# Kernel tuning notes

Hardware: AMD Instinct MI355X
Metric: run time of the kernel (lower is better)

Reference implementation:

```python
import jax, jax.numpy as jnp
import numpy as np

B, S = 2, 256
CN, CE = 256, 128        # node / edge channels
A, H, V = 32, 8, 32      # attention_size, heads, value_size
AH, VH = A * H, V * H


def setup_inputs() -> dict:
    key = jax.random.key(0)
    ks = jax.random.split(key, 16)
    w = lambda k, shape: (jax.random.normal(k, shape) * 0.05).astype(jnp.float32)
    nodes = jax.random.normal(ks[0], (B, CN, S), dtype=jnp.float32)
    edges = jax.random.normal(ks[1], (B, CE, S, S), dtype=jnp.float32)
    lengths = jnp.array([S, (3 * S) // 4])            # padded-batch valid lengths
    mask = jnp.arange(S)[None, :] < lengths[:, None]  # (B, S) bool
    return dict(
        nodes=nodes, edges=edges, mask=mask,
        Wq=w(ks[2], (AH, CN)),
        Wk=w(ks[3], (AH, CN + CE)),
        Wv=w(ks[4], (VH, CN + CE)),
        Wo=w(ks[5], (CN, VH)),
        We=w(ks[6], (CE, VH + CE)),
        Wm1=w(ks[7], (CN, CN)), bm1=jnp.zeros((CN,), jnp.float32),
        Wm2=w(ks[8], (CN, CN)), bm2=jnp.zeros((CN,), jnp.float32),
        We1=w(ks[9], (CE, CE)), be1=jnp.zeros((CE,), jnp.float32),
        We2=w(ks[10], (CE, CE)), be2=jnp.zeros((CE,), jnp.float32),
        an0=(jax.random.normal(ks[11], (CN,)) * 0.1).astype(jnp.float32),
        an1=(jax.random.normal(ks[12], (CN,)) * 0.1).astype(jnp.float32),
        ae0=(jax.random.normal(ks[13], (CE,)) * 0.1).astype(jnp.float32),
        ae1=(jax.random.normal(ks[14], (CE,)) * 0.1).astype(jnp.float32),
    )


def _block(nodes, edges, mask, Wq, Wk, Wv, Wo, We,
           Wm1, bm1, Wm2, bm2, We1, be1, We2, be2, an0, an1, ae0, ae1):
    relu = jax.nn.relu
    b, _, s = nodes.shape
    # node MLP (1x1 conv, ReLU, 1x1 conv, ReLU) + ReZero residual; dropout in eval mode = identity
    h = relu(jnp.einsum('oc,bcs->bos', Wm1, nodes) + bm1[None, :, None])
    h = relu(jnp.einsum('oc,bcs->bos', Wm2, h) + bm2[None, :, None])
    nodes = nodes + an0[None, :, None] * h
    # edge MLP (1x1 conv2d) + ReZero residual
    g = relu(jnp.einsum('oc,bcij->boij', We1, edges) + be1[None, :, None, None])
    g = relu(jnp.einsum('oc,bcij->boij', We2, g) + be2[None, :, None, None])
    edges = edges + ae0[None, :, None, None] * g
    # materialized multi-head attention
    q = jnp.einsum('ac,bcs->bas', Wq, nodes).reshape(b, H, A, s)            # (B,H,A,S)
    ne = jnp.concatenate([jnp.broadcast_to(nodes[:, :, :, None], (b, CN, s, s)), edges], axis=1)
    k = jnp.einsum('ac,bcij->baij', Wk, ne).reshape(b, H, A, s, s)          # (B,H,A,S,S)
    v = jnp.einsum('vc,bcij->bvij', Wv, ne).reshape(b, H, V, s, s)          # (B,H,V,S,S)
    sim = jnp.einsum('bhai,bhaij->bhij', q, k) / jnp.sqrt(jnp.float32(A))   # (B,H,S,S)
    sim = jnp.where(mask[:, None, None, :], sim, jnp.float32(-1e9))
    sim = jax.nn.softmax(sim, axis=-1)
    mm = (mask[:, None, None, :] & mask[:, None, :, None]).astype(sim.dtype)  # (B,1,S,S)
    sim = sim * mm
    v = v * mm[:, None]
    nf = jnp.einsum('bhij,bhvij->bhvi', sim, v).reshape(b, H * V, s)        # (B,HV,S)
    node_att = jnp.einsum('oc,bcs->bos', Wo, nf)
    # edge features: broadcast node features along j, symmetrize via transpose+average
    ef = 0.5 * (nf[:, :, :, None] + nf[:, :, None, :])                      # (B,HV,S,S)
    edge_att = jnp.einsum('oc,bcij->boij', We, jnp.concatenate([ef, edges], axis=1))
    # ReZero residuals (project_* are Identity since in_size == out_size)
    nodes = nodes + an1[None, :, None] * node_att
    edges = edges + ae1[None, :, None, None] * edge_att
    # final masking
    nodes = nodes * mask[:, None, :].astype(nodes.dtype)
    edges = edges * mm
    return nodes, edges


def reference(nodes, edges, mask, Wq, Wk, Wv, Wo, We, Wm1, bm1, Wm2, bm2,
              We1, be1, We2, be2, an0, an1, ae0, ae1):
    return _block(nodes, edges, mask, Wq, Wk, Wv, Wo, We,
                  Wm1, bm1, Wm2, bm2, We1, be1, We2, be2, an0, an1, ae0, ae1)
```

## Files before the change

kernel.cpp:

```cpp
#include <hip/hip_runtime.h>
#include <hip/hip_bf16.h>
#include <cstdint>
#include <cstddef>

constexpr int B_  = 2;
constexpr int S_  = 256;
constexpr int CN_ = 256;
constexpr int CE_ = 128;
constexpr int A_  = 32;
constexpr int H_  = 8;
constexpr int V_  = 32;
constexpr int AH_ = A_ * H_;
constexpr int VH_ = V_ * H_;
constexpr int SS_ = S_ * S_;
constexpr int CNE_ = CN_ + CE_;

constexpr size_t OFF_N1   = 0;
constexpr size_t OFF_Q    = OFF_N1  + (size_t)B_*CN_*S_;
constexpr size_t OFF_VN   = OFF_Q   + (size_t)B_*AH_*S_;
constexpr size_t OFF_NF   = OFF_VN  + (size_t)B_*VH_*S_;
constexpr size_t OFF_WNF  = OFF_NF  + (size_t)B_*VH_*S_;
constexpr size_t OFF_SE   = OFF_WNF + (size_t)B_*CE_*S_;
constexpr size_t OFF_QW   = OFF_SE  + (size_t)B_*S_*1024;
constexpr size_t OFF_WB1  = OFF_QW  + (size_t)B_*S_*1024;
constexpr size_t OFF_WB2  = OFF_WB1 + 16384;
constexpr size_t OFF_WBE  = OFF_WB2 + 16384;
constexpr size_t OFF_MASK = OFF_WBE + 16384;

__device__ inline uint16_t f2bf(float x) {
    uint32_t u = __float_as_uint(x);
    uint32_t r = (u + 0x7fffu + ((u >> 16) & 1u)) >> 16;
    return (uint16_t)r;
}
__device__ inline float bf2f(uint16_t h) {
    return __uint_as_float(((uint32_t)h) << 16);
}
__device__ inline uint32_t pack_split(float v) {
    uint32_t u  = __float_as_uint(v);
    uint32_t hm = u & 0xffff0000u;
    return hm | (__float_as_uint(v - __uint_as_float(hm)) >> 16);
}
__device__ inline float unpack_f32(uint32_t p) {
    return __uint_as_float(p & 0xffff0000u) + __uint_as_float(p << 16);
}

typedef __attribute__((ext_vector_type(8))) short sh8;
typedef __attribute__((ext_vector_type(4))) short sh4;
typedef __attribute__((ext_vector_type(4))) float f32x4;

#define MFMA_B16(a, b, c) __builtin_amdgcn_mfma_f32_16x16x32_bf16((a), (b), (c), 0, 0, 0)

__device__ inline int eidx(int j, int c) {
    return (j * 136 + c) ^ (((j >> 3) & 7) << 3);
}

#define GEMM4_K256(WROW, XS, A0, A1, A2, A3)                                   \
    for (int c = 0; c < 256; c += 4) {                                         \
        float4 w  = *(const float4*)((WROW) + c);                              \
        float4 x0 = *(const float4*)((XS) + (c+0)*4);                          \
        float4 x1 = *(const float4*)((XS) + (c+1)*4);                          \
        float4 x2 = *(const float4*)((XS) + (c+2)*4);                          \
        float4 x3 = *(const float4*)((XS) + (c+3)*4);                          \
        A0 = fmaf(w.x,x0.x,fmaf(w.y,x1.x,fmaf(w.z,x2.x,fmaf(w.w,x3.x,A0))));   \
        A1 = fmaf(w.x,x0.y,fmaf(w.y,x1.y,fmaf(w.z,x2.y,fmaf(w.w,x3.y,A1))));   \
        A2 = fmaf(w.x,x0.z,fmaf(w.y,x1.z,fmaf(w.z,x2.z,fmaf(w.w,x3.z,A2))));   \
        A3 = fmaf(w.x,x0.w,fmaf(w.y,x1.w,fmaf(w.z,x2.w,fmaf(w.w,x3.w,A3))));   \
    }

__global__ void k_mask_norm(const unsigned char* __restrict__ mraw,
                            float* __restrict__ ws)
{
    int t = threadIdx.x;
    unsigned char b1 = mraw[1], b2 = mraw[2];
    float mv;
    if (b1 == (unsigned char)1) {
        mv = mraw[t] ? 1.f : 0.f;
    } else if (b2 == (unsigned char)128) {
        mv = (((const float*)mraw)[t] != 0.f) ? 1.f : 0.f;
    } else {
        mv = (((const int*)mraw)[t] != 0) ? 1.f : 0.f;
    }
    ws[OFF_MASK + t] = mv;
}

__global__ void k_wprep(const float* __restrict__ We1_,
                        const float* __restrict__ We2_,
                        const float* __restrict__ We_,
                        float* __restrict__ ws)
{
    int idx = blockIdx.x * 256 + threadIdx.x;
    int m = idx >> 14;
    int r = idx & 16383;
    int o = r >> 7, c = r & 127;
    ushort* wb1 = (ushort*)(ws + OFF_WB1);
    ushort* wb2 = (ushort*)(ws + OFF_WB2);
    ushort* wbe = (ushort*)(ws + OFF_WBE);
    if (m == 0)      wb1[r] = f2bf(We1_[o*CE_ + c]);
    else if (m == 1) wb2[r] = f2bf(We2_[o*CE_ + c]);
    else             wbe[r] = f2bf(We_[o*CNE_ + CN_ + c]);
}

__global__ __launch_bounds__(256)
void k_node_mlp_qv(const float* __restrict__ nodes,
                   const float* __restrict__ Wm1, const float* __restrict__ bm1,
                   const float* __restrict__ Wm2, const float* __restrict__ bm2,
                   const float* __restrict__ an0,
                   const float* __restrict__ Wq,  const float* __restrict__ Wv,
                   float* __restrict__ ws)
{
    __shared__ float xs[CN_ * 4];
    __shared__ float hs[CN_ * 4];
    const int t  = threadIdx.x;
    const int b  = blockIdx.x >> 6;
    const int s0 = (blockIdx.x & 63) * 4;

    {
        float4 nv = *(const float4*)(nodes + (size_t)(b*CN_+t)*S_ + s0);
        xs[t*4+0]=nv.x; xs[t*4+1]=nv.y; xs[t*4+2]=nv.z; xs[t*4+3]=nv.w;
    }
    __syncthreads();

    float a0, a1, a2, a3;
    {
        float bv = bm1[t]; a0=bv; a1=bv; a2=bv; a3=bv;
        GEMM4_K256(Wm1 + t*CN_, xs, a0, a1, a2, a3);
        hs[t*4+0]=fmaxf(a0,0.f); hs[t*4+1]=fmaxf(a1,0.f);
        hs[t*4+2]=fmaxf(a2,0.f); hs[t*4+3]=fmaxf(a3,0.f);
    }
    __syncthreads();
    {
        float bv = bm2[t]; a0=bv; a1=bv; a2=bv; a3=bv;
        GEMM4_K256(Wm2 + t*CN_, hs, a0, a1, a2, a3);
    }
    {
        float an = an0[t];
        float n0 = xs[t*4+0] + an*fmaxf(a0,0.f);
        float n1 = xs[t*4+1] + an*fmaxf(a1,0.f);
        float n2 = xs[t*4+2] + an*fmaxf(a2,0.f);
        float n3 = xs[t*4+3] + an*fmaxf(a3,0.f);
        xs[t*4+0]=n0; xs[t*4+1]=n1; xs[t*4+2]=n2; xs[t*4+3]=n3;
        *(float4*)(ws + OFF_N1 + (size_t)(b*CN_+t)*S_ + s0) = make_float4(n0,n1,n2,n3);
    }
    __syncthreads();

    {
        a0=0.f; a1=0.f; a2=0.f; a3=0.f;
        GEMM4_K256(Wq + t*CN_, xs, a0, a1, a2, a3);
        const float rsA = 0.1767766952966369f;
        *(float4*)(ws + OFF_Q + (size_t)(b*AH_+t)*S_ + s0) =
            make_float4(a0*rsA, a1*rsA, a2*rsA, a3*rsA);
    }
    {
        a0=0.f; a1=0.f; a2=0.f; a3=0.f;
        GEMM4_K256(Wv + t*CNE_, xs, a0, a1, a2, a3);
        *(float4*)(ws + OFF_VN + (size_t)(b*VH_+t)*S_ + s0) = make_float4(a0,a1,a2,a3);
    }
}

__global__ __launch_bounds__(256)
void k_qw(float* __restrict__ ws, const float* __restrict__ Wk)
{
    __shared__ float qcol[AH_];
    const int t = threadIdx.x;
    const int b = blockIdx.x >> 8, i = blockIdx.x & 255;
    qcol[t] = ws[OFF_Q + (size_t)(b*AH_+t)*S_ + i];
    __syncthreads();
    const int c  = t & 127;
    const int h0 = (t >> 7) * 4;
    float acc[4] = {0.f, 0.f, 0.f, 0.f};
    for (int aa = 0; aa < A_; ++aa) {
        #pragma unroll
        for (int k = 0; k < 4; ++k) {
            int ha = (h0 + k)*A_ + aa;
            acc[k] = fmaf(qcol[ha], Wk[(size_t)ha*CNE_ + CN_ + c], acc[k]);
        }
    }
    float* q = ws + OFF_QW + (size_t)(b*S_ + i)*1024;
    #pragma unroll
    for (int k = 0; k < 4; ++k) q[c*8 + h0 + k] = acc[k];
}

__global__ __launch_bounds__(256, 2)
void k_edge_mlp(const float* __restrict__ edges,
                const float* __restrict__ ws,
                const float* __restrict__ be1, const float* __restrict__ be2,
                const float* __restrict__ ae0,
                uint32_t* __restrict__ e1out)
{
    __shared__ ushort Ehi[64 * 136];
    __shared__ ushort Elo[64 * 136];
    __shared__ ushort Ht [64 * 136];

    const int t  = threadIdx.x;
    const int b  = blockIdx.x >> 10;
    const int i  = (blockIdx.x >> 2) & 255;
    const int j0 = (blockIdx.x & 3) * 64;
    const float* Eb = edges + (size_t)b*CE_*SS_ + (size_t)i*S_ + j0;

    {
        const int tj = t & 15;
        const int p0 = t >> 4;
        #pragma unroll
        for (int s = 0; s < 4; ++s) {
            int c = (s*16 + p0) * 2;
            float4 v0 = *(const float4*)(Eb + (size_t)c*SS_ + tj*4);
            float4 v1 = *(const float4*)(Eb + (size_t)(c+1)*SS_ + tj*4);
            float q0[4] = {v0.x, v0.y, v0.z, v0.w};
            float q1[4] = {v1.x, v1.y, v1.z, v1.w};
            #pragma unroll
            for (int jj = 0; jj < 4; ++jj) {
                int j = tj*4 + jj;
                uint32_t u0 = __float_as_uint(q0[jj]), u1 = __float_as_uint(q1[jj]);
                uint32_t h0m = u0 & 0xffff0000u, h1m = u1 & 0xffff0000u;
                uint32_t hiw = (u0 >> 16) | h1m;
                uint32_t low = (__float_as_uint(q0[jj] - __uint_as_float(h0m)) >> 16)
                             | (__float_as_uint(q1[jj] - __uint_as_float(h1m)) & 0xffff0000u);
                int us = eidx(j, c);
                *(uint32_t*)&Ehi[us] = hiw;
                *(uint32_t*)&Elo[us] = low;
            }
        }
    }

    const int w  = t >> 6;
    const int l  = t & 63;
    const int lr = l & 15;
    const int lk = l >> 4;
    const ushort* wb1 = (const ushort*)(ws + OFF_WB1);
    const ushort* wb2 = (const ushort*)(ws + OFF_WB2);
    sh8 A1[2][4], A2[2][4];
    #pragma unroll
    for (int mt = 0; mt < 2; ++mt) {
        int o = w*32 + mt*16 + lr;
        #pragma unroll
        for (int ks = 0; ks < 4; ++ks) {
            A1[mt][ks] = *(const sh8*)(wb1 + o*CE_ + ks*32 + lk*8);
            A2[mt][ks] = *(const sh8*)(wb2 + o*CE_ + ks*32 + lk*8);
        }
    }

    f32x4 acc1[2][4];
    #pragma unroll
    for (int mt = 0; mt < 2; ++mt) {
        float4 bv = *(const float4*)(be1 + w*32 + mt*16 + lk*4);
        #pragma unroll
        for (int nt = 0; nt < 4; ++nt) {
            acc1[mt][nt][0] = bv.x; acc1[mt][nt][1] = bv.y;
            acc1[mt][nt][2] = bv.z; acc1[mt][nt][3] = bv.w;
        }
    }
    __syncthreads();
    #pragma unroll
    for (int nt = 0; nt < 4; ++nt) {
        int j = nt*16 + lr;
        sh8 bh[4], bl[4];
        #pragma unroll
        for (int ks = 0; ks < 4; ++ks) {
            int us = eidx(j, ks*32 + lk*8);
            bh[ks] = *(const sh8*)&Ehi[us];
            bl[ks] = *(const sh8*)&Elo[us];
        }
        #pragma unroll
        for (int mt = 0; mt < 2; ++mt)
            #pragma unroll
            for (int ks = 0; ks < 4; ++ks) {
                acc1[mt][nt] = MFMA_B16(A1[mt][ks], bh[ks], acc1[mt][nt]);
                acc1[mt][nt] = MFMA_B16(A1[mt][ks], bl[ks], acc1[mt][nt]);
            }
    }

    #pragma unroll
    for (int mt = 0; mt < 2; ++mt)
        #pragma unroll
        for (int nt = 0; nt < 4; ++nt) {
            int o0 = w*32 + mt*16 + lk*4;
            int j  = nt*16 + lr;
            uint32_t u0 = __float_as_uint(fmaxf(acc1[mt][nt][0], 0.f));
            uint32_t u1 = __float_as_uint(fmaxf(acc1[mt][nt][1], 0.f));
            uint32_t u2 = __float_as_uint(fmaxf(acc1[mt][nt][2], 0.f));
            uint32_t u3 = __float_as_uint(fmaxf(acc1[mt][nt][3], 0.f));
            int us = eidx(j, o0);
            *(uint32_t*)&Ht[us]     = (u0 >> 16) | (u1 & 0xffff0000u);
            *(uint32_t*)&Ht[us + 2] = (u2 >> 16) | (u3 & 0xffff0000u);
        }
    __syncthreads();

    f32x4 acc2[2][4];
    #pragma unroll
    for (int mt = 0; mt < 2; ++mt) {
        float4 bv = *(const float4*)(be2 + w*32 + mt*16 + lk*4);
        #pragma unroll
        for (int nt = 0; nt < 4; ++nt) {
            acc2[mt][nt][0] = bv.x; acc2[mt][nt][1] = bv.y;
            acc2[mt][nt][2] = bv.z; acc2[mt][nt][3] = bv.w;
        }
    }
    #pragma unroll
    for (int nt = 0; nt < 4; ++nt) {
        int j = nt*16 + lr;
        sh8 hh[4];
        #pragma unroll
        for (int ks = 0; ks < 4; ++ks)
            hh[ks] = *(const sh8*)&Ht[eidx(j, ks*32 + lk*8)];
        #pragma unroll
        for (int mt = 0; mt < 2; ++mt)
            #pragma unroll
            for (int ks = 0; ks < 4; ++ks)
                acc2[mt][nt] = MFMA_B16(A2[mt][ks], hh[ks], acc2[mt][nt]);
    }

    #pragma unroll
    for (int mt = 0; mt < 2; ++mt) {
        int o0 = w*32 + mt*16 + lk*4;
        float4 a0v = *(const float4*)(ae0 + o0);
        float aev[4] = {a0v.x, a0v.y, a0v.z, a0v.w};
        #pragma unroll
        for (int nt = 0; nt < 4; ++nt) {
            int j = nt*16 + lr;
            int us = eidx(j, o0);
            sh4 eh = *(const sh4*)&Ehi[us];
            sh4 el = *(const sh4*)&Elo[us];
            #pragma unroll
            for (int r = 0; r < 4; ++r) {
                float e = bf2f((uint16_t)eh[r]) + bf2f((uint16_t)el[r]);
                float g = fmaxf(acc2[mt][nt][r], 0.f);
                e1out[(size_t)(b*CE_ + o0 + r)*SS_ + (size_t)i*S_ + j0 + j] =
                    pack_split(e + aev[r]*g);
            }
        }
    }
}

__global__ __launch_bounds__(256)
void k_attn(const uint32_t* __restrict__ e1, float* __restrict__ ws)
{
    __shared__ float qw[CE_ * 8];
    __shared__ float simL[H_ * S_];
    __shared__ float Etile[CE_ * 65];
    const int t = threadIdx.x;
    const int b = blockIdx.x >> 8, i = blockIdx.x & 255;
    const float* maskf = ws + OFF_MASK;

    {
        const float4* qwg = (const float4*)(ws + OFF_QW + (size_t)(b*S_ + i)*1024);
        ((float4*)qw)[t] = qwg[t];
    }
    __syncthreads();

    const uint32_t* Eb = e1 + ((size_t)(b*CE_)*S_ + i)*S_;
    float sv[8];
    #pragma unroll
    for (int h = 0; h < 8; ++h) sv[h] = 0.f;
    for (int c = 0; c < CE_; ++c) {
        float e = unpack_f32(Eb[(size_t)c*SS_ + t]);
        float4 q0 = *(const float4*)(qw + c*8);
        float4 q1 = *(const float4*)(qw + c*8 + 4);
        sv[0] = fmaf(q0.x, e, sv[0]); sv[1] = fmaf(q0.y, e, sv[1]);
        sv[2] = fmaf(q0.z, e, sv[2]); sv[3] = fmaf(q0.w, e, sv[3]);
        sv[4] = fmaf(q1.x, e, sv[4]); sv[5] = fmaf(q1.y, e, sv[5]);
        sv[6] = fmaf(q1.z, e, sv[6]); sv[7] = fmaf(q1.w, e, sv[7]);
    }
    const bool mj = maskf[b*S_ + t] != 0.f;
    #pragma unroll
    for (int h = 0; h < 8; ++h) simL[h*S_ + t] = mj ? sv[h] : -1e9f;
    __syncthreads();

    {
        const int h = t >> 5, l = t & 31;
        float vv[8]; float m = -3.4e38f;
        #pragma unroll
        for (int k = 0; k < 8; ++k) { vv[k] = simL[h*S_ + l + k*32]; m = fmaxf(m, vv[k]); }
        #pragma unroll
        for (int off = 16; off >= 1; off >>= 1) m = fmaxf(m, __shfl_xor(m, off, 32));
        float ssum = 0.f; float ex[8];
        #pragma unroll
        for (int k = 0; k < 8; ++k) { ex[k] = __expf(vv[k] - m); ssum += ex[k]; }
        #pragma unroll
        for (int off = 16; off >= 1; off >>= 1) ssum += __shfl_xor(ssum, off, 32);
        const float mi = maskf[b*S_ + i];
        const float rr = mi / ssum;
        #pragma unroll
        for (int k = 0; k < 8; ++k) simL[h*S_ + l + k*32] = ex[k] * rr;
    }
    __syncthreads();

    const int cp = t & 127, hg = t >> 7;
    float a4[4] = {0.f, 0.f, 0.f, 0.f};
    for (int jt = 0; jt < 4; ++jt) {
        #pragma unroll 4
        for (int r = 0; r < 32; ++r) {
            int idx = r*256 + t;
            int c = idx >> 6, j = idx & 63;
            Etile[c*65 + j] = unpack_f32(Eb[(size_t)c*SS_ + jt*64 + j]);
        }
        __syncthreads();
        for (int j = 0; j < 64; ++j) {
            float e = Etile[cp*65 + j];
            #pragma unroll
            for (int k = 0; k < 4; ++k)
                a4[k] = fmaf(e, simL[(hg*4+k)*S_ + jt*64 + j], a4[k]);
        }
        __syncthreads();
    }
    float* se = ws + OFF_SE + (size_t)(b*S_ + i)*1024;
    #pragma unroll
    for (int k = 0; k < 4; ++k) se[(hg*4+k)*128 + cp] = a4[k];
}

__global__ __launch_bounds__(256)
void k_nf(float* __restrict__ ws, const float* __restrict__ Wv)
{
    __shared__ float seL[1024];
    const int t = threadIdx.x;
    const int b = blockIdx.x >> 8, i = blockIdx.x & 255;
    const float* se = ws + OFF_SE + (size_t)(b*S_ + i)*1024;
    #pragma unroll
    for (int k = 0; k < 4; ++k) seL[k*256 + t] = se[k*256 + t];
    __syncthreads();
    const int h = t >> 5;
    float acc = 0.f;
    for (int c = 0; c < CE_; ++c)
        acc = fmaf(Wv[t*CNE_ + CN_ + c], seL[h*128 + c], acc);
    const float mi = ws[OFF_MASK + b*S_ + i];
    float nfv = ws[OFF_VN + ((size_t)(b*VH_+t))*S_ + i] * mi + acc;
    ws[OFF_NF + ((size_t)(b*VH_+t))*S_ + i] = nfv;
}

__global__ __launch_bounds__(256)
void k_node_out(float* __restrict__ ws, const float* __restrict__ Wo,
                const float* __restrict__ We, const float* __restrict__ an1,
                float* __restrict__ out_nodes)
{
    __shared__ float xs[VH_ * 4];
    const int t  = threadIdx.x;
    const int b  = blockIdx.x >> 6;
    const int s0 = (blockIdx.x & 63) * 4;
    {
        float4 nv = *(const float4*)(ws + OFF_NF + (size_t)(b*VH_+t)*S_ + s0);
        xs[t*4+0]=nv.x; xs[t*4+1]=nv.y; xs[t*4+2]=nv.z; xs[t*4+3]=nv.w;
    }
    __syncthreads();
    float a0=0.f, a1=0.f, a2=0.f, a3=0.f;
    GEMM4_K256(Wo + t*VH_, xs, a0, a1, a2, a3);
    {
        float aw = an1[t];
        float4 n1 = *(const float4*)(ws + OFF_N1 + (size_t)(b*CN_+t)*S_ + s0);
        float4 mk = *(const float4*)(ws + OFF_MASK + b*S_ + s0);
        *(float4*)(out_nodes + (size_t)(b*CN_+t)*S_ + s0) = make_float4(
            (n1.x + aw*a0) * mk.x, (n1.y + aw*a1) * mk.y,
            (n1.z + aw*a2) * mk.z, (n1.w + aw*a3) * mk.w);
    }
    if (t < CE_) {
        a0=0.f; a1=0.f; a2=0.f; a3=0.f;
        GEMM4_K256(We + t*CNE_, xs, a0, a1, a2, a3);
        *(float4*)(ws + OFF_WNF + (size_t)(b*CE_+t)*S_ + s0) = make_float4(a0,a1,a2,a3);
    }
}

__global__ __launch_bounds__(256, 2)
void k_edge_out(const uint32_t* __restrict__ e1p, float* __restrict__ e1f,
                const float* __restrict__ ws, const float* __restrict__ ae1)
{
    __shared__ ushort Ehi[64 * 136];
    __shared__ ushort Elo[64 * 136];
    __shared__ float  wni_s[CE_];

    const int t  = threadIdx.x;
    const int b  = blockIdx.x >> 10;
    const int i  = (blockIdx.x >> 2) & 255;
    const int j0 = (blockIdx.x & 3) * 64;
    const uint32_t* Ebp = e1p + (size_t)b*CE_*SS_ + (size_t)i*S_ + j0;
    float*          Ebf = e1f + (size_t)b*CE_*SS_ + (size_t)i*S_ + j0;
    const float* Wnf   = ws + OFF_WNF;
    const float* maskf = ws + OFF_MASK;

    if (t < CE_) wni_s[t] = Wnf[(size_t)(b*CE_ + t)*S_ + i];

    {
        const int tj = t & 15;
        const int p0 = t >> 4;
        #pragma unroll
        for (int s = 0; s < 4; ++s) {
            int c = (s*16 + p0) * 2;
            uint4 v0 = *(const uint4*)(Ebp + (size_t)c*SS_ + tj*4);
            uint4 v1 = *(const uint4*)(Ebp + (size_t)(c+1)*SS_ + tj*4);
            uint32_t w0[4] = {v0.x, v0.y, v0.z, v0.w};
            uint32_t w1[4] = {v1.x, v1.y, v1.z, v1.w};
            #pragma unroll
            for (int jj = 0; jj < 4; ++jj) {
                int j = tj*4 + jj;
                int us = eidx(j, c);
                *(uint32_t*)&Ehi[us] = (w0[jj] >> 16) | (w1[jj] & 0xffff0000u);
                *(uint32_t*)&Elo[us] = (w0[jj] & 0xffffu) | (w1[jj] << 16);
            }
        }
    }

    const int w  = t >> 6;
    const int l  = t & 63;
    const int lr = l & 15;
    const int lk = l >> 4;
    const ushort* wbe = (const ushort*)(ws + OFF_WBE);
    sh8 AE[2][4];
    #pragma unroll
    for (int mt = 0; mt < 2; ++mt) {
        int o = w*32 + mt*16 + lr;
        #pragma unroll
        for (int ks = 0; ks < 4; ++ks)
            AE[mt][ks] = *(const sh8*)(wbe + o*CE_ + ks*32 + lk*8);
    }

    f32x4 acc[2][4];
    #pragma unroll
    for (int mt = 0; mt < 2; ++mt)
        #pragma unroll
        for (int nt = 0; nt < 4; ++nt)
            acc[mt][nt] = (f32x4){0.f, 0.f, 0.f, 0.f};
    __syncthreads();
    #pragma unroll
    for (int nt = 0; nt < 4; ++nt) {
        int j = nt*16 + lr;
        sh8 bh[4], bl[4];
        #pragma unroll
        for (int ks = 0; ks < 4; ++ks) {
            int us = eidx(j, ks*32 + lk*8);
            bh[ks] = *(const sh8*)&Ehi[us];
            bl[ks] = *(const sh8*)&Elo[us];
        }
        #pragma unroll
        for (int mt = 0; mt < 2; ++mt)
            #pragma unroll
            for (int ks = 0; ks < 4; ++ks) {
                acc[mt][nt] = MFMA_B16(AE[mt][ks], bh[ks], acc[mt][nt]);
                acc[mt][nt] = MFMA_B16(AE[mt][ks], bl[ks], acc[mt][nt]);
            }
    }

    const float mi = maskf[b*S_ + i];
    #pragma unroll
    for (int mt = 0; mt < 2; ++mt) {
        int o0 = w*32 + mt*16 + lk*4;
        float4 a1v = *(const float4*)(ae1 + o0);
        float aev[4] = {a1v.x, a1v.y, a1v.z, a1v.w};
        #pragma unroll
        for (int nt = 0; nt < 4; ++nt) {
            int j  = nt*16 + lr;
            int jg = j0 + j;
            float mj = maskf[b*S_ + jg];
            int us = eidx(j, o0);
            sh4 eh = *(const sh4*)&Ehi[us];
            sh4 el = *(const sh4*)&Elo[us];
            #pragma unroll
            for (int r = 0; r < 4; ++r) {
                float e   = bf2f((uint16_t)eh[r]) + bf2f((uint16_t)el[r]);
                float att = 0.5f*(wni_s[o0+r] + Wnf[(size_t)(b*CE_+o0+r)*S_ + jg])
                          + acc[mt][nt][r];
                Ebf[(size_t)(o0+r)*SS_ + j] = (e + aev[r]*att) * (mi * mj);
            }
        }
    }
}

extern "C" void kernel_launch(void* const* d_in, const int* in_sizes, int n_in,
                              void* d_out, int out_size, void* d_ws, size_t ws_size,
                              hipStream_t stream)
{
    const float* nodes = (const float*)d_in[0];
    const float* edges = (const float*)d_in[1];
    const unsigned char* mraw = (const unsigned char*)d_in[2];
    const float* Wq  = (const float*)d_in[3];
    const float* Wk  = (const float*)d_in[4];
    const float* Wv  = (const float*)d_in[5];
    const float* Wo  = (const float*)d_in[6];
    const float* We  = (const float*)d_in[7];
    const float* Wm1 = (const float*)d_in[8];
    const float* bm1 = (const float*)d_in[9];
    const float* Wm2 = (const float*)d_in[10];
    const float* bm2 = (const float*)d_in[11];
    const float* We1 = (const float*)d_in[12];
    const float* be1 = (const float*)d_in[13];
    const float* We2 = (const float*)d_in[14];
    const float* be2 = (const float*)d_in[15];
    const float* an0 = (const float*)d_in[16];
    const float* an1 = (const float*)d_in[17];
    const float* ae0 = (const float*)d_in[18];
    const float* ae1 = (const float*)d_in[19];

    float* ws = (float*)d_ws;
    float* out_nodes = (float*)d_out;
    float* out_edges = out_nodes + (size_t)B_*CN_*S_;

    k_mask_norm  <<<1,    512, 0, stream>>>(mraw, ws);
    k_wprep      <<<192,  256, 0, stream>>>(We1, We2, We, ws);
    k_node_mlp_qv<<<128,  256, 0, stream>>>(nodes, Wm1, bm1, Wm2, bm2, an0, Wq, Wv, ws);
    k_qw         <<<512,  256, 0, stream>>>(ws, Wk);
    k_edge_mlp   <<<2048, 256, 0, stream>>>(edges, ws, be1, be2, ae0, (uint32_t*)out_edges);
    k_attn       <<<512,  256, 0, stream>>>((const uint32_t*)out_edges, ws);
    k_nf         <<<512,  256, 0, stream>>>(ws, Wv);
    k_node_out   <<<128,  256, 0, stream>>>(ws, Wo, We, an1, out_nodes);
    k_edge_out   <<<2048, 256, 0, stream>>>((const uint32_t*)out_edges, out_edges, ws, ae1);
}
```

Before: 312.7 us.

## Fuse qW and nf projections into attention, drop low-half bf16 MFMAs

```diff
diff --git a/kernel.cpp b/kernel.cpp
--- a/kernel.cpp
+++ b/kernel.cpp
@@ -20,12 +20,11 @@
 constexpr size_t OFF_VN   = OFF_Q   + (size_t)B_*AH_*S_;
 constexpr size_t OFF_NF   = OFF_VN  + (size_t)B_*VH_*S_;
 constexpr size_t OFF_WNF  = OFF_NF  + (size_t)B_*VH_*S_;
-constexpr size_t OFF_SE   = OFF_WNF + (size_t)B_*CE_*S_;
-constexpr size_t OFF_QW   = OFF_SE  + (size_t)B_*S_*1024;
-constexpr size_t OFF_WB1  = OFF_QW  + (size_t)B_*S_*1024;
+constexpr size_t OFF_WB1  = OFF_WNF + (size_t)B_*CE_*S_;
 constexpr size_t OFF_WB2  = OFF_WB1 + 16384;
 constexpr size_t OFF_WBE  = OFF_WB2 + 16384;
-constexpr size_t OFF_MASK = OFF_WBE + 16384;
+constexpr size_t OFF_WKT  = OFF_WBE + 16384;
+constexpr size_t OFF_MASK = OFF_WKT + 32768;
 
 __device__ inline uint16_t f2bf(float x) {
     uint32_t u = __float_as_uint(x);
@@ -36,9 +35,9 @@
     return __uint_as_float(((uint32_t)h) << 16);
 }
 __device__ inline uint32_t pack_split(float v) {
-    uint32_t u  = __float_as_uint(v);
-    uint32_t hm = u & 0xffff0000u;
-    return hm | (__float_as_uint(v - __uint_as_float(hm)) >> 16);
+    uint32_t hi = (uint32_t)f2bf(v);
+    float res = v - __uint_as_float(hi << 16);
+    return (hi << 16) | (__float_as_uint(res) >> 16);
 }
 __device__ inline float unpack_f32(uint32_t p) {
     return __uint_as_float(p & 0xffff0000u) + __uint_as_float(p << 16);
@@ -86,18 +85,25 @@
 __global__ void k_wprep(const float* __restrict__ We1_,
                         const float* __restrict__ We2_,
                         const float* __restrict__ We_,
+                        const float* __restrict__ Wk_,
                         float* __restrict__ ws)
 {
     int idx = blockIdx.x * 256 + threadIdx.x;
     int m = idx >> 14;
-    int r = idx & 16383;
-    int o = r >> 7, c = r & 127;
-    ushort* wb1 = (ushort*)(ws + OFF_WB1);
-    ushort* wb2 = (ushort*)(ws + OFF_WB2);
-    ushort* wbe = (ushort*)(ws + OFF_WBE);
-    if (m == 0)      wb1[r] = f2bf(We1_[o*CE_ + c]);
-    else if (m == 1) wb2[r] = f2bf(We2_[o*CE_ + c]);
-    else             wbe[r] = f2bf(We_[o*CNE_ + CN_ + c]);
+    if (m < 3) {
+        int r = idx & 16383;
+        int o = r >> 7, c = r & 127;
+        ushort* wb1 = (ushort*)(ws + OFF_WB1);
+        ushort* wb2 = (ushort*)(ws + OFF_WB2);
+        ushort* wbe = (ushort*)(ws + OFF_WBE);
+        if (m == 0)      wb1[r] = f2bf(We1_[o*CE_ + c]);
+        else if (m == 1) wb2[r] = f2bf(We2_[o*CE_ + c]);
+        else             wbe[r] = f2bf(We_[o*CNE_ + CN_ + c]);
+    } else {
+        int r = idx - 49152;
+        int a = r >> 10, h = (r >> 7) & 7, c = r & 127;
+        ws[OFF_WKT + r] = Wk_[(size_t)(h*A_ + a)*CNE_ + CN_ + c];
+    }
 }
 
 __global__ __launch_bounds__(256)
@@ -157,29 +163,6 @@
     }
 }
 
-__global__ __launch_bounds__(256)
-void k_qw(float* __restrict__ ws, const float* __restrict__ Wk)
-{
-    __shared__ float qcol[AH_];
-    const int t = threadIdx.x;
-    const int b = blockIdx.x >> 8, i = blockIdx.x & 255;
-    qcol[t] = ws[OFF_Q + (size_t)(b*AH_+t)*S_ + i];
-    __syncthreads();
-    const int c  = t & 127;
-    const int h0 = (t >> 7) * 4;
-    float acc[4] = {0.f, 0.f, 0.f, 0.f};
-    for (int aa = 0; aa < A_; ++aa) {
-        #pragma unroll
-        for (int k = 0; k < 4; ++k) {
-            int ha = (h0 + k)*A_ + aa;
-            acc[k] = fmaf(qcol[ha], Wk[(size_t)ha*CNE_ + CN_ + c], acc[k]);
-        }
-    }
-    float* q = ws + OFF_QW + (size_t)(b*S_ + i)*1024;
-    #pragma unroll
-    for (int k = 0; k < 4; ++k) q[c*8 + h0 + k] = acc[k];
-}
-
 __global__ __launch_bounds__(256, 2)
 void k_edge_mlp(const float* __restrict__ edges,
                 const float* __restrict__ ws,
@@ -210,14 +193,14 @@
             #pragma unroll
             for (int jj = 0; jj < 4; ++jj) {
                 int j = tj*4 + jj;
-                uint32_t u0 = __float_as_uint(q0[jj]), u1 = __float_as_uint(q1[jj]);
-                uint32_t h0m = u0 & 0xffff0000u, h1m = u1 & 0xffff0000u;
-                uint32_t hiw = (u0 >> 16) | h1m;
-                uint32_t low = (__float_as_uint(q0[jj] - __uint_as_float(h0m)) >> 16)
-                             | (__float_as_uint(q1[jj] - __uint_as_float(h1m)) & 0xffff0000u);
+                uint32_t h0 = (uint32_t)f2bf(q0[jj]);
+                uint32_t h1 = (uint32_t)f2bf(q1[jj]);
+                float r0 = q0[jj] - __uint_as_float(h0 << 16);
+                float r1 = q1[jj] - __uint_as_float(h1 << 16);
                 int us = eidx(j, c);
-                *(uint32_t*)&Ehi[us] = hiw;
-                *(uint32_t*)&Elo[us] = low;
+                *(uint32_t*)&Ehi[us] = h0 | (h1 << 16);
+                *(uint32_t*)&Elo[us] = (__float_as_uint(r0) >> 16)
+                                     | (__float_as_uint(r1) & 0xffff0000u);
             }
         }
     }
@@ -253,20 +236,15 @@
     #pragma unroll
     for (int nt = 0; nt < 4; ++nt) {
         int j = nt*16 + lr;
-        sh8 bh[4], bl[4];
-        #pragma unroll
-        for (int ks = 0; ks < 4; ++ks) {
-            int us = eidx(j, ks*32 + lk*8);
-            bh[ks] = *(const sh8*)&Ehi[us];
-            bl[ks] = *(const sh8*)&Elo[us];
-        }
+        sh8 bh[4];
+        #pragma unroll
+        for (int ks = 0; ks < 4; ++ks)
+            bh[ks] = *(const sh8*)&Ehi[eidx(j, ks*32 + lk*8)];
         #pragma unroll
         for (int mt = 0; mt < 2; ++mt)
             #pragma unroll
-            for (int ks = 0; ks < 4; ++ks) {
+            for (int ks = 0; ks < 4; ++ks)
                 acc1[mt][nt] = MFMA_B16(A1[mt][ks], bh[ks], acc1[mt][nt]);
-                acc1[mt][nt] = MFMA_B16(A1[mt][ks], bl[ks], acc1[mt][nt]);
-            }
     }
 
     #pragma unroll
@@ -332,18 +310,33 @@
 }
 
 __global__ __launch_bounds__(256)
-void k_attn(const uint32_t* __restrict__ e1, float* __restrict__ ws)
-{
+void k_attn(const uint32_t* __restrict__ e1, float* __restrict__ ws,
+            const float* __restrict__ Wv)
+{
+    __shared__ float qcol[AH_];
     __shared__ float qw[CE_ * 8];
     __shared__ float simL[H_ * S_];
     __shared__ float Etile[CE_ * 65];
+    __shared__ float seL[1024];
     const int t = threadIdx.x;
     const int b = blockIdx.x >> 8, i = blockIdx.x & 255;
     const float* maskf = ws + OFF_MASK;
 
-    {
-        const float4* qwg = (const float4*)(ws + OFF_QW + (size_t)(b*S_ + i)*1024);
-        ((float4*)qw)[t] = qwg[t];
+    qcol[t] = ws[OFF_Q + (size_t)(b*AH_+t)*S_ + i];
+    __syncthreads();
+
+    {
+        const float* WkT = ws + OFF_WKT;
+        #pragma unroll
+        for (int k = 0; k < 4; ++k) {
+            int idx = k*256 + t;
+            int c = idx & 127, h = idx >> 7;
+            float acc = 0.f;
+            #pragma unroll 8
+            for (int aa = 0; aa < A_; ++aa)
+                acc = fmaf(qcol[h*A_ + aa], WkT[aa*1024 + h*128 + c], acc);
+            qw[c*8 + h] = acc;
+        }
     }
     __syncthreads();
 
@@ -402,28 +395,25 @@
         }
         __syncthreads();
     }
-    float* se = ws + OFF_SE + (size_t)(b*S_ + i)*1024;
-    #pragma unroll
-    for (int k = 0; k < 4; ++k) se[(hg*4+k)*128 + cp] = a4[k];
-}
-
-__global__ __launch_bounds__(256)
-void k_nf(float* __restrict__ ws, const float* __restrict__ Wv)
-{
-    __shared__ float seL[1024];
-    const int t = threadIdx.x;
-    const int b = blockIdx.x >> 8, i = blockIdx.x & 255;
-    const float* se = ws + OFF_SE + (size_t)(b*S_ + i)*1024;
-    #pragma unroll
-    for (int k = 0; k < 4; ++k) seL[k*256 + t] = se[k*256 + t];
-    __syncthreads();
-    const int h = t >> 5;
-    float acc = 0.f;
-    for (int c = 0; c < CE_; ++c)
-        acc = fmaf(Wv[t*CNE_ + CN_ + c], seL[h*128 + c], acc);
-    const float mi = ws[OFF_MASK + b*S_ + i];
-    float nfv = ws[OFF_VN + ((size_t)(b*VH_+t))*S_ + i] * mi + acc;
-    ws[OFF_NF + ((size_t)(b*VH_+t))*S_ + i] = nfv;
+    #pragma unroll
+    for (int k = 0; k < 4; ++k) seL[(hg*4+k)*128 + cp] = a4[k];
+    __syncthreads();
+
+    {
+        const int h2 = t >> 5;
+        float acc = 0.f;
+        const float* wvr = Wv + (size_t)t*CNE_ + CN_;
+        for (int c = 0; c < CE_; c += 4) {
+            float4 wv4 = *(const float4*)(wvr + c);
+            acc = fmaf(wv4.x, seL[h2*128 + c],     acc);
+            acc = fmaf(wv4.y, seL[h2*128 + c + 1], acc);
+            acc = fmaf(wv4.z, seL[h2*128 + c + 2], acc);
+            acc = fmaf(wv4.w, seL[h2*128 + c + 3], acc);
+        }
+        const float mi = maskf[b*S_ + i];
+        float nfv = ws[OFF_VN + (size_t)(b*VH_+t)*S_ + i] * mi + acc;
+        ws[OFF_NF + (size_t)(b*VH_+t)*S_ + i] = nfv;
+    }
 }
 
 __global__ __launch_bounds__(256)
@@ -520,20 +510,15 @@
     #pragma unroll
     for (int nt = 0; nt < 4; ++nt) {
         int j = nt*16 + lr;
-        sh8 bh[4], bl[4];
-        #pragma unroll
-        for (int ks = 0; ks < 4; ++ks) {
-            int us = eidx(j, ks*32 + lk*8);
-            bh[ks] = *(const sh8*)&Ehi[us];
-            bl[ks] = *(const sh8*)&Elo[us];
-        }
+        sh8 bh[4];
+        #pragma unroll
+        for (int ks = 0; ks < 4; ++ks)
+            bh[ks] = *(const sh8*)&Ehi[eidx(j, ks*32 + lk*8)];
         #pragma unroll
         for (int mt = 0; mt < 2; ++mt)
             #pragma unroll
-            for (int ks = 0; ks < 4; ++ks) {
+            for (int ks = 0; ks < 4; ++ks)
                 acc[mt][nt] = MFMA_B16(AE[mt][ks], bh[ks], acc[mt][nt]);
-                acc[mt][nt] = MFMA_B16(AE[mt][ks], bl[ks], acc[mt][nt]);
-            }
     }
 
     const float mi = maskf[b*S_ + i];
@@ -546,7 +531,7 @@
         for (int nt = 0; nt < 4; ++nt) {
             int j  = nt*16 + lr;
             int jg = j0 + j;
-            float mj = maskf[b*S_ + jg];
+            float mjv = maskf[b*S_ + jg];
             int us = eidx(j, o0);
             sh4 eh = *(const sh4*)&Ehi[us];
             sh4 el = *(const sh4*)&Elo[us];
@@ -555,7 +540,7 @@
                 float e   = bf2f((uint16_t)eh[r]) + bf2f((uint16_t)el[r]);
                 float att = 0.5f*(wni_s[o0+r] + Wnf[(size_t)(b*CE_+o0+r)*S_ + jg])
                           + acc[mt][nt][r];
-                Ebf[(size_t)(o0+r)*SS_ + j] = (e + aev[r]*att) * (mi * mj);
+                Ebf[(size_t)(o0+r)*SS_ + j] = (e + aev[r]*att) * (mi * mjv);
             }
         }
     }
@@ -591,12 +576,10 @@
     float* out_edges = out_nodes + (size_t)B_*CN_*S_;
 
     k_mask_norm  <<<1,    512, 0, stream>>>(mraw, ws);
-    k_wprep      <<<192,  256, 0, stream>>>(We1, We2, We, ws);
+    k_wprep      <<<320,  256, 0, stream>>>(We1, We2, We, Wk, ws);
     k_node_mlp_qv<<<128,  256, 0, stream>>>(nodes, Wm1, bm1, Wm2, bm2, an0, Wq, Wv, ws);
-    k_qw         <<<512,  256, 0, stream>>>(ws, Wk);
     k_edge_mlp   <<<2048, 256, 0, stream>>>(edges, ws, be1, be2, ae0, (uint32_t*)out_edges);
-    k_attn       <<<512,  256, 0, stream>>>((const uint32_t*)out_edges, ws);
-    k_nf         <<<512,  256, 0, stream>>>(ws, Wv);
+    k_attn       <<<512,  256, 0, stream>>>((const uint32_t*)out_edges, ws, Wv);
     k_node_out   <<<128,  256, 0, stream>>>(ws, Wo, We, an1, out_nodes);
     k_edge_out   <<<2048, 256, 0, stream>>>((const uint32_t*)out_edges, out_edges, ws, ae1);
 }
```

Measured after the change: 301.3 us. 1.04x faster.
